# Performance work log

Measured on AMD Instinct MI355X. Metric: run time of the kernel, lower is better.

## Reference

```python
import jax, jax.numpy as jnp
import numpy as np

EPS = 1e-6

def elu_feature_map(x):
    return jax.nn.elu(x) + 1.0

def setup_inputs() -> dict:
    key = jax.random.key(0)
    ks = jax.random.split(key, 5)
    B, S, D, H, Hd = 4, 4096, 1024, 16, 64
    scale = 1.0 / np.sqrt(D)
    x = jax.random.normal(ks[0], (B, S, D), dtype=jnp.float32)
    Wq = jax.random.normal(ks[1], (D, H, Hd), dtype=jnp.float32) * scale
    Wk = jax.random.normal(ks[2], (D, H, Hd), dtype=jnp.float32) * scale
    Wv = jax.random.normal(ks[3], (D, H, Hd), dtype=jnp.float32) * scale
    Wo = jax.random.normal(ks[4], (H, Hd, D), dtype=jnp.float32) * (1.0 / np.sqrt(H * Hd))
    bq = jnp.zeros((H, Hd), dtype=jnp.float32)
    bk = jnp.zeros((H, Hd), dtype=jnp.float32)
    bv = jnp.zeros((H, Hd), dtype=jnp.float32)
    bo = jnp.zeros((D,), dtype=jnp.float32)
    return {"x": x, "Wq": Wq, "bq": bq, "Wk": Wk, "bk": bk, "Wv": Wv, "bv": bv, "Wo": Wo, "bo": bo}

def reference(x, Wq, bq, Wk, bk, Wv, bv, Wo, bo):
    # QKV projections: [n,s,D] x [D,h,d] -> [n,s,h,d]
    q = jnp.einsum('nsD,Dhd->nshd', x, Wq) + bq
    k = jnp.einsum('nsD,Dhd->nshd', x, Wk) + bk
    v = jnp.einsum('nsD,Dhd->nshd', x, Wv) + bv
    qf = elu_feature_map(q)
    kf = elu_feature_map(k)
    # kv state per head: [n,h,m,d]
    kv = jnp.einsum('nshd,nshm->nhmd', kf, v)
    # normalizer: [n,l,h]
    z = 1.0 / (jnp.einsum('nlhd,nhd->nlh', qf, jnp.sum(kf, axis=1)) + EPS)
    # output: [n,l,h,m]
    y = jnp.einsum('nlhd,nhmd,nlh->nlhm', qf, kv, z)
    # output projection contracting (head, head_dim)
    out = jnp.einsum('nlhm,hmD->nlD', y, Wo) + bo
    return out
```

## Files before the change

### kernel.cpp

```cpp
#include <hip/hip_runtime.h>
#include <cstddef>
#include <cstdint>


typedef __attribute__((ext_vector_type(8))) __bf16 bf16x8;
typedef __attribute__((ext_vector_type(4))) __bf16 bf16x4;
typedef __attribute__((ext_vector_type(2))) __bf16 bf16x2;
typedef __attribute__((ext_vector_type(4))) float f32x4;

__device__ __forceinline__ void async_cp16(const void* g, void* s) {
    __builtin_amdgcn_global_load_lds(
        (__attribute__((address_space(1))) void*)g,
        (__attribute__((address_space(3))) void*)s, 16, 0, 0);
}

__device__ __forceinline__ void mfma_core(const __bf16* __restrict__ A,
                                          const __bf16* __restrict__ BT,
                                          int mbase, int nbase,
                                          __bf16* As, __bf16* Bs,
                                          f32x4 acc[4][4])
{
    const int t    = threadIdx.x;
    const int lane = t & 63;
    const int wid  = t >> 6;
    const int wm   = (wid >> 1) * 64;
    const int wn   = (wid & 1) * 64;
    const int fr   = lane & 15;
    const int fq   = lane >> 4;
    const int srow = lane >> 2;
    const int skof = (lane & 3) * 8;

    const __bf16* arow0 = A  + (size_t)(mbase + wid * 32 + srow) * 1024 + skof;
    const __bf16* brow0 = BT + (size_t)(nbase + wid * 32 + srow) * 1024 + skof;

    for (int kt = 0; kt < 1024; kt += 32) {
        async_cp16(arow0 + kt,             As + (2 * wid + 0) * 512);
        async_cp16(arow0 + kt + 16 * 1024, As + (2 * wid + 1) * 512);
        async_cp16(brow0 + kt,             Bs + (2 * wid + 0) * 512);
        async_cp16(brow0 + kt + 16 * 1024, Bs + (2 * wid + 1) * 512);
        __syncthreads();

        bf16x8 af[4], bfr[4];
#pragma unroll
        for (int i = 0; i < 4; i++) {
            af[i]  = *(const bf16x8*)(As + (wm + i * 16 + fr) * 32 + fq * 8);
            bfr[i] = *(const bf16x8*)(Bs + (wn + i * 16 + fr) * 32 + fq * 8);
        }
#pragma unroll
        for (int i = 0; i < 4; i++)
#pragma unroll
            for (int j = 0; j < 4; j++)
                acc[i][j] = __builtin_amdgcn_mfma_f32_16x16x32_bf16(
                    af[i], bfr[j], acc[i][j], 0, 0, 0);
        __syncthreads();
    }
}

__global__ __launch_bounds__(256) void gemm_qkv_mfma(
    const __bf16* __restrict__ xb,
    const __bf16* __restrict__ wqt, const __bf16* __restrict__ wkt,
    const __bf16* __restrict__ wvt,
    const float* __restrict__ bq, const float* __restrict__ bk,
    const float* __restrict__ bv,
    __bf16* __restrict__ qfb, __bf16* __restrict__ kfb, __bf16* __restrict__ vb)
{
    __shared__ __bf16 As[128 * 32];
    __shared__ __bf16 Bs[128 * 32];
    f32x4 acc[4][4];
#pragma unroll
    for (int i = 0; i < 4; i++)
#pragma unroll
        for (int j = 0; j < 4; j++) acc[i][j] = (f32x4){0.f, 0.f, 0.f, 0.f};

    const int mt = blockIdx.x;
    const int nt = blockIdx.y;
    const int which = nt >> 3;
    const int nbase = (nt & 7) * 128;
    const int mbase = mt * 128;

    const __bf16* BT  = (which == 0) ? wqt : (which == 1) ? wkt : wvt;
    const float* bias = (which == 0) ? bq : (which == 1) ? bk : bv;
    __bf16* outp      = (which == 0) ? qfb : (which == 1) ? kfb : vb;
    const bool feat   = (which < 2);

    mfma_core(xb, BT, mbase, nbase, As, Bs, acc);

    const int t = threadIdx.x, lane = t & 63, wid = t >> 6;
    const int wm = (wid >> 1) * 64, wn = (wid & 1) * 64;
    const int fr = lane & 15, fq = lane >> 4;

#pragma unroll
    for (int i = 0; i < 4; i++)
#pragma unroll
        for (int j = 0; j < 4; j++) {
            const int col = nbase + wn + j * 16 + fr;
            const float bval = bias[col];
#pragma unroll
            for (int r = 0; r < 4; r++) {
                const int row = mbase + wm + i * 16 + fq * 4 + r;
                float vv = acc[i][j][r] + bval;
                if (feat) vv = (vv > 0.f) ? (vv + 1.f) : __expf(vv);
                outp[(size_t)row * 1024 + col] = (__bf16)vv;
            }
        }
}

__global__ __launch_bounds__(256) void gemm_out_mfma(
    const __bf16* __restrict__ yb, const __bf16* __restrict__ wot,
    const float* __restrict__ bo, float* __restrict__ out)
{
    __shared__ __bf16 As[128 * 32];
    __shared__ __bf16 Bs[128 * 32];
    f32x4 acc[4][4];
#pragma unroll
    for (int i = 0; i < 4; i++)
#pragma unroll
        for (int j = 0; j < 4; j++) acc[i][j] = (f32x4){0.f, 0.f, 0.f, 0.f};

    const int mbase = blockIdx.x * 128;
    const int nbase = blockIdx.y * 128;

    mfma_core(yb, wot, mbase, nbase, As, Bs, acc);

    const int t = threadIdx.x, lane = t & 63, wid = t >> 6;
    const int wm = (wid >> 1) * 64, wn = (wid & 1) * 64;
    const int fr = lane & 15, fq = lane >> 4;

#pragma unroll
    for (int i = 0; i < 4; i++)
#pragma unroll
        for (int j = 0; j < 4; j++) {
            const int col = nbase + wn + j * 16 + fr;
            const float bval = bo[col];
#pragma unroll
            for (int r = 0; r < 4; r++) {
                const int row = mbase + wm + i * 16 + fq * 4 + r;
                out[(size_t)row * 1024 + col] = acc[i][j][r] + bval;
            }
        }
}

__global__ __launch_bounds__(256) void kv_ksum_mfma(
    const __bf16* __restrict__ kfb, const __bf16* __restrict__ vb,
    float* __restrict__ kvp, float* __restrict__ ksp)
{
    __shared__ __bf16 kfs[64 * 66];
    __shared__ __bf16 vs[64 * 66];

    const int bh = blockIdx.x;
    const int n = bh >> 4, h = bh & 15;
    const int chunk = blockIdx.y;
    const int t = threadIdx.x, lane = t & 63, w = t >> 6;
    const int fr = lane & 15, fq = lane >> 4;

    f32x4 acc[4];
#pragma unroll
    for (int j = 0; j < 4; j++) acc[j] = (f32x4){0.f, 0.f, 0.f, 0.f};
    f32x4 accks = (f32x4){0.f, 0.f, 0.f, 0.f};

    bf16x8 ones;
#pragma unroll
    for (int e = 0; e < 8; e++) ones[e] = (__bf16)1.0f;

    const size_t base = ((size_t)n * 4096 + (size_t)chunk * 256) * 1024 + h * 64;

    for (int tile = 0; tile < 4; tile++) {
#pragma unroll
        for (int i = 0; i < 2; i++) {
            int idx = t + i * 256;
            int s = idx >> 3, d0 = (idx & 7) * 8;
            bf16x8 k8 = *(const bf16x8*)(kfb + base + (size_t)(tile * 64 + s) * 1024 + d0);
            bf16x8 v8 = *(const bf16x8*)(vb  + base + (size_t)(tile * 64 + s) * 1024 + d0);
#pragma unroll
            for (int e = 0; e < 4; e++) {
                *(bf16x2*)(kfs + s * 66 + d0 + 2 * e) = (bf16x2){k8[2*e], k8[2*e+1]};
                *(bf16x2*)(vs  + s * 66 + d0 + 2 * e) = (bf16x2){v8[2*e], v8[2*e+1]};
            }
        }
        __syncthreads();

#pragma unroll
        for (int kk = 0; kk < 2; kk++) {
            bf16x8 af, bfr[4];
#pragma unroll
            for (int j = 0; j < 8; j++)
                af[j] = vs[(kk * 32 + fq * 8 + j) * 66 + 16 * w + fr];
#pragma unroll
            for (int j2 = 0; j2 < 4; j2++)
#pragma unroll
                for (int j = 0; j < 8; j++)
                    bfr[j2][j] = kfs[(kk * 32 + fq * 8 + j) * 66 + 16 * j2 + fr];
#pragma unroll
            for (int j2 = 0; j2 < 4; j2++)
                acc[j2] = __builtin_amdgcn_mfma_f32_16x16x32_bf16(
                    af, bfr[j2], acc[j2], 0, 0, 0);
            accks = __builtin_amdgcn_mfma_f32_16x16x32_bf16(
                ones, bfr[w], accks, 0, 0, 0);
        }
        __syncthreads();
    }

    const size_t pbase = ((size_t)bh * 16 + chunk) * 4096;
#pragma unroll
    for (int j2 = 0; j2 < 4; j2++)
#pragma unroll
        for (int r = 0; r < 4; r++) {
            int m = 16 * w + fq * 4 + r;
            int d = 16 * j2 + fr;
            kvp[pbase + m * 64 + d] = acc[j2][r];
        }
    if (fq == 0)
        ksp[((size_t)bh * 16 + chunk) * 64 + 16 * w + fr] = accks[0];
}

__global__ __launch_bounds__(256) void reduce_kv(
    const float* __restrict__ kvp, const float* __restrict__ ksp,
    __bf16* __restrict__ kvb, __bf16* __restrict__ ksumb)
{
    const int b = blockIdx.x;
    if (b < 1024) {
        int i = b * 256 + threadIdx.x;
        int bh = i >> 12, md = i & 4095;
        float s = 0.f;
#pragma unroll
        for (int c = 0; c < 16; c++) s += kvp[((size_t)bh * 16 + c) * 4096 + md];
        kvb[i] = (__bf16)s;
    } else {
        int j = (b - 1024) * 256 + threadIdx.x;
        int bh = j >> 6, d = j & 63;
        float s = 0.f;
#pragma unroll
        for (int c = 0; c < 16; c++) s += ksp[((size_t)bh * 16 + c) * 64 + d];
        ksumb[j] = (__bf16)s;
    }
}

__global__ __launch_bounds__(256) void y_mfma(
    const __bf16* __restrict__ qfb, const __bf16* __restrict__ kvb,
    const __bf16* __restrict__ ksumb, __bf16* __restrict__ yb)
{
    __shared__ __bf16 qs[128 * 72];
    __shared__ __bf16 kvs[64 * 72];

    const int gbase = blockIdx.x * 128;
    const int h = blockIdx.y;
    const int bh = (gbase >> 12) * 16 + h;
    const int t = threadIdx.x, lane = t & 63, w = t >> 6;
    const int fr = lane & 15, fq = lane >> 4;

#pragma unroll
    for (int i = 0; i < 4; i++) {
        int idx = t + i * 256;
        int l = idx >> 3, d0 = (idx & 7) * 8;
        *(bf16x8*)(qs + l * 72 + d0) =
            *(const bf16x8*)(qfb + (size_t)(gbase + l) * 1024 + h * 64 + d0);
    }
#pragma unroll
    for (int i = 0; i < 2; i++) {
        int idx = t + i * 256;
        int m = idx >> 3, d0 = (idx & 7) * 8;
        *(bf16x8*)(kvs + m * 72 + d0) =
            *(const bf16x8*)(kvb + (size_t)bh * 4096 + m * 64 + d0);
    }
    bf16x8 ksb[2];
#pragma unroll
    for (int kk = 0; kk < 2; kk++)
        ksb[kk] = *(const bf16x8*)(ksumb + bh * 64 + kk * 32 + fq * 8);
    __syncthreads();

    f32x4 acc[2][4], accz[2];
#pragma unroll
    for (int i = 0; i < 2; i++) {
        accz[i] = (f32x4){0.f, 0.f, 0.f, 0.f};
#pragma unroll
        for (int j = 0; j < 4; j++) acc[i][j] = (f32x4){0.f, 0.f, 0.f, 0.f};
    }

#pragma unroll
    for (int kk = 0; kk < 2; kk++) {
        bf16x8 af[2], bfr[4];
#pragma unroll
        for (int i = 0; i < 2; i++)
            af[i] = *(const bf16x8*)(qs + (32 * w + 16 * i + fr) * 72 + kk * 32 + fq * 8);
#pragma unroll
        for (int j = 0; j < 4; j++)
            bfr[j] = *(const bf16x8*)(kvs + (16 * j + fr) * 72 + kk * 32 + fq * 8);
#pragma unroll
        for (int i = 0; i < 2; i++) {
#pragma unroll
            for (int j = 0; j < 4; j++)
                acc[i][j] = __builtin_amdgcn_mfma_f32_16x16x32_bf16(
                    af[i], bfr[j], acc[i][j], 0, 0, 0);
            accz[i] = __builtin_amdgcn_mfma_f32_16x16x32_bf16(
                af[i], ksb[kk], accz[i], 0, 0, 0);
        }
    }

#pragma unroll
    for (int i = 0; i < 2; i++)
#pragma unroll
        for (int r = 0; r < 4; r++) {
            const float z = 1.0f / (accz[i][r] + 1e-6f);
            const int g = gbase + 32 * w + 16 * i + fq * 4 + r;
#pragma unroll
            for (int j = 0; j < 4; j++)
                yb[(size_t)g * 1024 + h * 64 + 16 * j + fr] =
                    (__bf16)(acc[i][j][r] * z);
        }
}

__global__ __launch_bounds__(256) void cast_x(const float* __restrict__ x,
                                              __bf16* __restrict__ xb)
{
    const size_t i = ((size_t)blockIdx.x * 256 + threadIdx.x) * 8;
    float4 a = *(const float4*)(x + i);
    float4 b = *(const float4*)(x + i + 4);
    bf16x8 o;
    o[0] = (__bf16)a.x; o[1] = (__bf16)a.y; o[2] = (__bf16)a.z; o[3] = (__bf16)a.w;
    o[4] = (__bf16)b.x; o[5] = (__bf16)b.y; o[6] = (__bf16)b.z; o[7] = (__bf16)b.w;
    *(bf16x8*)(xb + i) = o;
}

__global__ __launch_bounds__(256) void transpose_w(
    const float* __restrict__ w0, const float* __restrict__ w1,
    const float* __restrict__ w2, const float* __restrict__ w3,
    __bf16* __restrict__ o0, __bf16* __restrict__ o1,
    __bf16* __restrict__ o2, __bf16* __restrict__ o3)
{
    __shared__ float ld[32][33];
    const int wsel = blockIdx.z;
    const float* src = (wsel == 0) ? w0 : (wsel == 1) ? w1 : (wsel == 2) ? w2 : w3;
    __bf16* dst      = (wsel == 0) ? o0 : (wsel == 1) ? o1 : (wsel == 2) ? o2 : o3;

    const int kbase = blockIdx.x * 32;
    const int nbase = blockIdx.y * 32;
    const int t = threadIdx.x;
    const int r = t >> 3, c4 = (t & 7) * 4;

    float4 a = *(const float4*)(src + (size_t)(kbase + r) * 1024 + nbase + c4);
    ld[r][c4 + 0] = a.x; ld[r][c4 + 1] = a.y; ld[r][c4 + 2] = a.z; ld[r][c4 + 3] = a.w;
    __syncthreads();

    bf16x4 o;
    o[0] = (__bf16)ld[c4 + 0][r];
    o[1] = (__bf16)ld[c4 + 1][r];
    o[2] = (__bf16)ld[c4 + 2][r];
    o[3] = (__bf16)ld[c4 + 3][r];
    *(bf16x4*)(dst + (size_t)(nbase + r) * 1024 + kbase + c4) = o;
}

extern "C" void kernel_launch(void* const* d_in, const int* in_sizes, int n_in,
                              void* d_out, int out_size, void* d_ws, size_t ws_size,
                              hipStream_t stream)
{
    const float* x  = (const float*)d_in[0];
    const float* Wq = (const float*)d_in[1];
    const float* bq = (const float*)d_in[2];
    const float* Wk = (const float*)d_in[3];
    const float* bk = (const float*)d_in[4];
    const float* Wv = (const float*)d_in[5];
    const float* bv = (const float*)d_in[6];
    const float* Wo = (const float*)d_in[7];
    const float* bo = (const float*)d_in[8];
    float* out = (float*)d_out;

    __bf16* xb    = (__bf16*)d_ws;
    __bf16* wqt   = xb + (size_t)16777216;
    __bf16* wkt   = wqt + 1048576;
    __bf16* wvt   = wkt + 1048576;
    __bf16* wot   = wvt + 1048576;
    __bf16* qfb   = wot + 1048576;
    __bf16* kfb   = qfb + (size_t)16777216;
    __bf16* vb    = kfb + (size_t)16777216;
    float*  kvp   = (float*)(vb + (size_t)16777216);
    float*  ksp   = kvp + 4194304;
    __bf16* kvb   = (__bf16*)(ksp + 65536);
    __bf16* ksumb = kvb + 262144;

    cast_x<<<dim3(8192), dim3(256), 0, stream>>>(x, xb);
    transpose_w<<<dim3(32, 32, 4), dim3(256), 0, stream>>>(
        Wq, Wk, Wv, Wo, wqt, wkt, wvt, wot);

    gemm_qkv_mfma<<<dim3(128, 24), dim3(256), 0, stream>>>(
        xb, wqt, wkt, wvt, bq, bk, bv, qfb, kfb, vb);
    kv_ksum_mfma<<<dim3(64, 16), dim3(256), 0, stream>>>(kfb, vb, kvp, ksp);
    reduce_kv<<<dim3(1040), dim3(256), 0, stream>>>(kvp, ksp, kvb, ksumb);
    y_mfma<<<dim3(128, 16), dim3(256), 0, stream>>>(qfb, kvb, ksumb, kfb);
    gemm_out_mfma<<<dim3(128, 8), dim3(256), 0, stream>>>(kfb, wot, bo, out);
}
```

Measured before the change: 359.3 us.

## Replace 128x128 GEMM core with double-buffered swizzled 256x256 MFMA pipeline

Rewrites the shared GEMM core used by the QKV and output projections to compute 256x256 tiles with 8 waves and a k-step of 64. The A and B slabs are double-buffered in 128 KB of dynamic LDS via async global-to-LDS copies. LDS rows are XOR-swizzled to avoid bank conflicts, and MFMA quadrants are interleaved with fragment loads and prefetches of later tiles, using priority hints. This aims to raise data reuse and overlap memory with compute, at the cost of higher register pressure and fewer blocks for the output GEMM.

```diff
diff --git a/kernel.cpp b/kernel.cpp
--- a/kernel.cpp
+++ b/kernel.cpp
@@ -14,49 +14,144 @@
         (__attribute__((address_space(3))) void*)s, 16, 0, 0);
 }
 
-__device__ __forceinline__ void mfma_core(const __bf16* __restrict__ A,
-                                          const __bf16* __restrict__ BT,
-                                          int mbase, int nbase,
-                                          __bf16* As, __bf16* Bs,
-                                          f32x4 acc[4][4])
-{
+
+#define QUAD(ARR, BRR, RO, CO)                                                 \
+    _Pragma("unroll")                                                          \
+    for (int _qi = 0; _qi < 4; ++_qi)                                          \
+        _Pragma("unroll")                                                      \
+        for (int _qj = 0; _qj < 2; ++_qj)                                      \
+            _Pragma("unroll")                                                  \
+            for (int _qk = 0; _qk < 2; ++_qk)                                  \
+                acc[(RO) + _qi][(CO) + _qj] =                                  \
+                    __builtin_amdgcn_mfma_f32_16x16x32_bf16(                   \
+                        ARR[_qi][_qk], BRR[_qj][_qk],                          \
+                        acc[(RO) + _qi][(CO) + _qj], 0, 0, 0);
+
+__device__ __forceinline__ void mfma256_core(const __bf16* __restrict__ A,
+                                             const __bf16* __restrict__ BT,
+                                             int mbase, int nbase,
+                                             f32x4 acc[8][4])
+{
+    extern __shared__ __bf16 lds[];
+    constexpr int NT = 16;
     const int t    = threadIdx.x;
     const int lane = t & 63;
     const int wid  = t >> 6;
-    const int wm   = (wid >> 1) * 64;
-    const int wn   = (wid & 1) * 64;
+    const int wm   = wid >> 2;
+    const int wn   = wid & 3;
     const int fr   = lane & 15;
     const int fq   = lane >> 4;
-    const int srow = lane >> 2;
-    const int skof = (lane & 3) * 8;
-
-    const __bf16* arow0 = A  + (size_t)(mbase + wid * 32 + srow) * 1024 + skof;
-    const __bf16* brow0 = BT + (size_t)(nbase + wid * 32 + srow) * 1024 + skof;
-
-    for (int kt = 0; kt < 1024; kt += 32) {
-        async_cp16(arow0 + kt,             As + (2 * wid + 0) * 512);
-        async_cp16(arow0 + kt + 16 * 1024, As + (2 * wid + 1) * 512);
-        async_cp16(brow0 + kt,             Bs + (2 * wid + 0) * 512);
-        async_cp16(brow0 + kt + 16 * 1024, Bs + (2 * wid + 1) * 512);
-        __syncthreads();
-
-        bf16x8 af[4], bfr[4];
-#pragma unroll
-        for (int i = 0; i < 4; i++) {
-            af[i]  = *(const bf16x8*)(As + (wm + i * 16 + fr) * 32 + fq * 8);
-            bfr[i] = *(const bf16x8*)(Bs + (wn + i * 16 + fr) * 32 + fq * 8);
-        }
-#pragma unroll
-        for (int i = 0; i < 4; i++)
-#pragma unroll
-            for (int j = 0; j < 4; j++)
-                acc[i][j] = __builtin_amdgcn_mfma_f32_16x16x32_bf16(
-                    af[i], bfr[j], acc[i][j], 0, 0, 0);
-        __syncthreads();
-    }
-}
-
-__global__ __launch_bounds__(256) void gemm_qkv_mfma(
+    const int srow  = lane >> 3;
+    const int sslot = ((lane & 7) ^ srow) << 3;
+
+    const __bf16* aBase = A  + (size_t)mbase * 1024;
+    const __bf16* bBase = BT + (size_t)nbase * 1024;
+
+#define STAGE_A(tile)                                                          \
+    { const int _b = (tile) & 1;                                               \
+      _Pragma("unroll") for (int _h = 0; _h < 2; ++_h)                         \
+      _Pragma("unroll") for (int _i = 0; _i < 2; ++_i) {                       \
+          const int _c = 2 * wid + _i;                                         \
+          async_cp16(aBase + (size_t)(_h * 128 + _c * 8 + srow) * 1024         \
+                         + (tile) * 64 + sslot,                                \
+                     lds + _b * 32768 + _h * 8192 + _c * 512); } }
+#define STAGE_B(tile)                                                          \
+    { const int _b = (tile) & 1;                                               \
+      _Pragma("unroll") for (int _h = 0; _h < 2; ++_h)                         \
+      _Pragma("unroll") for (int _i = 0; _i < 2; ++_i) {                       \
+          const int _c = 2 * wid + _i;                                         \
+          async_cp16(bBase + (size_t)(_h * 128 + _c * 8 + srow) * 1024         \
+                         + (tile) * 64 + sslot,                                \
+                     lds + _b * 32768 + 16384 + _h * 8192 + _c * 512); } }
+#define LDA(ri, ks, b)                                                         \
+    (*(const bf16x8*)(lds + (b) * 32768 + (wm * 128 + (ri) * 16 + fr) * 64     \
+                      + (((ks) * 32 + fq * 8) ^ ((fr & 7) << 3))))
+#define LDB(cj, ks, b)                                                         \
+    (*(const bf16x8*)(lds + (b) * 32768 + 16384                                \
+                      + (wn * 64 + (cj) * 16 + fr) * 64                        \
+                      + (((ks) * 32 + fq * 8) ^ ((fr & 7) << 3))))
+
+    bf16x8 aR0[4][2], aR1[4][2], bC0[2][2], bC1[2][2];
+
+    STAGE_A(0) STAGE_B(0) STAGE_A(1) STAGE_B(1)
+    asm volatile("s_waitcnt vmcnt(8)" ::: "memory");
+    __builtin_amdgcn_s_barrier();
+
+#pragma unroll
+    for (int i = 0; i < 4; ++i)
+#pragma unroll
+        for (int ks = 0; ks < 2; ++ks) aR0[i][ks] = LDA(i, ks, 0);
+#pragma unroll
+    for (int j = 0; j < 2; ++j)
+#pragma unroll
+        for (int ks = 0; ks < 2; ++ks) bC0[j][ks] = LDB(j, ks, 0);
+
+    for (int T = 0; T < NT; ++T) {
+        const int bc = T & 1, bn = bc ^ 1;
+
+#pragma unroll
+        for (int i = 0; i < 4; ++i)
+#pragma unroll
+            for (int ks = 0; ks < 2; ++ks) aR1[i][ks] = LDA(4 + i, ks, bc);
+        __builtin_amdgcn_s_barrier();
+        asm volatile("s_waitcnt lgkmcnt(0)" ::: "memory");
+        __builtin_amdgcn_sched_barrier(0);
+        __builtin_amdgcn_s_setprio(1);
+        QUAD(aR0, bC0, 0, 0)
+        __builtin_amdgcn_s_setprio(0);
+        __builtin_amdgcn_s_barrier();
+
+        asm volatile("s_waitcnt vmcnt(4)" ::: "memory");
+#pragma unroll
+        for (int j = 0; j < 2; ++j)
+#pragma unroll
+            for (int ks = 0; ks < 2; ++ks) bC1[j][ks] = LDB(2 + j, ks, bc);
+        if (T + 2 < NT) STAGE_A(T + 2)
+        __builtin_amdgcn_s_barrier();
+        asm volatile("s_waitcnt lgkmcnt(0)" ::: "memory");
+        __builtin_amdgcn_sched_barrier(0);
+        __builtin_amdgcn_s_setprio(1);
+        QUAD(aR0, bC1, 0, 2)
+        __builtin_amdgcn_s_setprio(0);
+        __builtin_amdgcn_s_barrier();
+
+        asm volatile("s_waitcnt vmcnt(4)" ::: "memory");
+        if (T + 1 < NT) {
+#pragma unroll
+            for (int i = 0; i < 4; ++i)
+#pragma unroll
+                for (int ks = 0; ks < 2; ++ks) aR0[i][ks] = LDA(i, ks, bn);
+        }
+        if (T + 2 < NT) STAGE_B(T + 2)
+        __builtin_amdgcn_s_barrier();
+        asm volatile("s_waitcnt lgkmcnt(0)" ::: "memory");
+        __builtin_amdgcn_sched_barrier(0);
+        __builtin_amdgcn_s_setprio(1);
+        QUAD(aR1, bC0, 4, 0)
+        __builtin_amdgcn_s_setprio(0);
+        __builtin_amdgcn_s_barrier();
+
+        if (T + 1 < NT) {
+#pragma unroll
+            for (int j = 0; j < 2; ++j)
+#pragma unroll
+                for (int ks = 0; ks < 2; ++ks) bC0[j][ks] = LDB(j, ks, bn);
+        }
+        __builtin_amdgcn_s_barrier();
+        asm volatile("s_waitcnt lgkmcnt(0)" ::: "memory");
+        __builtin_amdgcn_sched_barrier(0);
+        __builtin_amdgcn_s_setprio(1);
+        QUAD(aR1, bC1, 4, 2)
+        __builtin_amdgcn_s_setprio(0);
+        __builtin_amdgcn_s_barrier();
+    }
+#undef STAGE_A
+#undef STAGE_B
+#undef LDA
+#undef LDB
+}
+
+__global__ __launch_bounds__(512) void gemm_qkv_256(
     const __bf16* __restrict__ xb,
     const __bf16* __restrict__ wqt, const __bf16* __restrict__ wkt,
     const __bf16* __restrict__ wvt,
@@ -64,78 +159,74 @@
     const float* __restrict__ bv,
     __bf16* __restrict__ qfb, __bf16* __restrict__ kfb, __bf16* __restrict__ vb)
 {
-    __shared__ __bf16 As[128 * 32];
-    __shared__ __bf16 Bs[128 * 32];
-    f32x4 acc[4][4];
-#pragma unroll
-    for (int i = 0; i < 4; i++)
-#pragma unroll
-        for (int j = 0; j < 4; j++) acc[i][j] = (f32x4){0.f, 0.f, 0.f, 0.f};
+    f32x4 acc[8][4];
+#pragma unroll
+    for (int i = 0; i < 8; ++i)
+#pragma unroll
+        for (int j = 0; j < 4; ++j) acc[i][j] = (f32x4){0.f, 0.f, 0.f, 0.f};
 
     const int mt = blockIdx.x;
     const int nt = blockIdx.y;
-    const int which = nt >> 3;
-    const int nbase = (nt & 7) * 128;
-    const int mbase = mt * 128;
+    const int which = nt >> 2;
+    const int nbase = (nt & 3) * 256;
+    const int mbase = mt * 256;
 
     const __bf16* BT  = (which == 0) ? wqt : (which == 1) ? wkt : wvt;
     const float* bias = (which == 0) ? bq : (which == 1) ? bk : bv;
     __bf16* outp      = (which == 0) ? qfb : (which == 1) ? kfb : vb;
     const bool feat   = (which < 2);
 
-    mfma_core(xb, BT, mbase, nbase, As, Bs, acc);
+    mfma256_core(xb, BT, mbase, nbase, acc);
 
     const int t = threadIdx.x, lane = t & 63, wid = t >> 6;
-    const int wm = (wid >> 1) * 64, wn = (wid & 1) * 64;
+    const int wm = wid >> 2, wn = wid & 3;
     const int fr = lane & 15, fq = lane >> 4;
 
 #pragma unroll
-    for (int i = 0; i < 4; i++)
-#pragma unroll
-        for (int j = 0; j < 4; j++) {
-            const int col = nbase + wn + j * 16 + fr;
+    for (int ri = 0; ri < 8; ++ri)
+#pragma unroll
+        for (int cj = 0; cj < 4; ++cj) {
+            const int col = nbase + wn * 64 + cj * 16 + fr;
             const float bval = bias[col];
 #pragma unroll
-            for (int r = 0; r < 4; r++) {
-                const int row = mbase + wm + i * 16 + fq * 4 + r;
-                float vv = acc[i][j][r] + bval;
+            for (int r = 0; r < 4; ++r) {
+                const int row = mbase + wm * 128 + ri * 16 + fq * 4 + r;
+                float vv = acc[ri][cj][r] + bval;
                 if (feat) vv = (vv > 0.f) ? (vv + 1.f) : __expf(vv);
                 outp[(size_t)row * 1024 + col] = (__bf16)vv;
             }
         }
 }
 
-__global__ __launch_bounds__(256) void gemm_out_mfma(
+__global__ __launch_bounds__(512) void gemm_out_256(
     const __bf16* __restrict__ yb, const __bf16* __restrict__ wot,
     const float* __restrict__ bo, float* __restrict__ out)
 {
-    __shared__ __bf16 As[128 * 32];
-    __shared__ __bf16 Bs[128 * 32];
-    f32x4 acc[4][4];
-#pragma unroll
-    for (int i = 0; i < 4; i++)
-#pragma unroll
-        for (int j = 0; j < 4; j++) acc[i][j] = (f32x4){0.f, 0.f, 0.f, 0.f};
-
-    const int mbase = blockIdx.x * 128;
-    const int nbase = blockIdx.y * 128;
-
-    mfma_core(yb, wot, mbase, nbase, As, Bs, acc);
+    f32x4 acc[8][4];
+#pragma unroll
+    for (int i = 0; i < 8; ++i)
+#pragma unroll
+        for (int j = 0; j < 4; ++j) acc[i][j] = (f32x4){0.f, 0.f, 0.f, 0.f};
+
+    const int mbase = blockIdx.x * 256;
+    const int nbase = blockIdx.y * 256;
+
+    mfma256_core(yb, wot, mbase, nbase, acc);
 
     const int t = threadIdx.x, lane = t & 63, wid = t >> 6;
-    const int wm = (wid >> 1) * 64, wn = (wid & 1) * 64;
+    const int wm = wid >> 2, wn = wid & 3;
     const int fr = lane & 15, fq = lane >> 4;
 
 #pragma unroll
-    for (int i = 0; i < 4; i++)
-#pragma unroll
-        for (int j = 0; j < 4; j++) {
-            const int col = nbase + wn + j * 16 + fr;
+    for (int ri = 0; ri < 8; ++ri)
+#pragma unroll
+        for (int cj = 0; cj < 4; ++cj) {
+            const int col = nbase + wn * 64 + cj * 16 + fr;
             const float bval = bo[col];
 #pragma unroll
-            for (int r = 0; r < 4; r++) {
-                const int row = mbase + wm + i * 16 + fq * 4 + r;
-                out[(size_t)row * 1024 + col] = acc[i][j][r] + bval;
+            for (int r = 0; r < 4; ++r) {
+                const int row = mbase + wm * 128 + ri * 16 + fq * 4 + r;
+                out[(size_t)row * 1024 + col] = acc[ri][cj][r] + bval;
             }
         }
 }
@@ -377,14 +468,20 @@
     __bf16* kvb   = (__bf16*)(ksp + 65536);
     __bf16* ksumb = kvb + 262144;
 
+    const int LDS_BYTES = 131072;
+    (void)hipFuncSetAttribute((const void*)gemm_qkv_256,
+                              hipFuncAttributeMaxDynamicSharedMemorySize, LDS_BYTES);
+    (void)hipFuncSetAttribute((const void*)gemm_out_256,
+                              hipFuncAttributeMaxDynamicSharedMemorySize, LDS_BYTES);
+
     cast_x<<<dim3(8192), dim3(256), 0, stream>>>(x, xb);
     transpose_w<<<dim3(32, 32, 4), dim3(256), 0, stream>>>(
         Wq, Wk, Wv, Wo, wqt, wkt, wvt, wot);
 
-    gemm_qkv_mfma<<<dim3(128, 24), dim3(256), 0, stream>>>(
+    gemm_qkv_256<<<dim3(64, 12), dim3(512), LDS_BYTES, stream>>>(
         xb, wqt, wkt, wvt, bq, bk, bv, qfb, kfb, vb);
     kv_ksum_mfma<<<dim3(64, 16), dim3(256), 0, stream>>>(kfb, vb, kvp, ksp);
     reduce_kv<<<dim3(1040), dim3(256), 0, stream>>>(kvp, ksp, kvb, ksumb);
     y_mfma<<<dim3(128, 16), dim3(256), 0, stream>>>(qfb, kvb, ksumb, kfb);
-    gemm_out_mfma<<<dim3(128, 8), dim3(256), 0, stream>>>(kfb, wot, bo, out);
-}
+    gemm_out_256<<<dim3(64, 4), dim3(512), LDS_BYTES, stream>>>(kfb, wot, bo, out);
+}
```

After: 327.3 us. -8.9%, faster.
